# Optimization experiments

Measured on AMD Instinct MI355X. Metric: run time of the kernel, lower is better.

The kernel has to match this reference:

```python
import jax, jax.numpy as jnp
import numpy as np

EMBED = 1024
HEADS = 16
HEAD_DIM = EMBED // HEADS


def setup_inputs() -> dict:
    key = jax.random.key(0)
    ks = jax.random.split(key, 9)
    s = 1.0 / np.sqrt(EMBED)
    inp = {
        "x": jax.random.normal(ks[0], (2, 2048, EMBED), dtype=jnp.float32),
        "wq": jax.random.uniform(ks[1], (EMBED, EMBED), jnp.float32, -s, s),
        "bq": jax.random.uniform(ks[2], (EMBED,), jnp.float32, -s, s),
        "wk": jax.random.uniform(ks[3], (EMBED, EMBED), jnp.float32, -s, s),
        "bk": jax.random.uniform(ks[4], (EMBED,), jnp.float32, -s, s),
        "wv": jax.random.uniform(ks[5], (EMBED, EMBED), jnp.float32, -s, s),
        "bv": jax.random.uniform(ks[6], (EMBED,), jnp.float32, -s, s),
        "wo": jax.random.uniform(ks[7], (EMBED, EMBED), jnp.float32, -s, s),
        "bo": jax.random.uniform(ks[8], (EMBED,), jnp.float32, -s, s),
    }
    return inp


def reference(x, wq, bq, wk, bk, wv, bv, wo, bo):
    B, S, E = x.shape
    H, D = HEADS, HEAD_DIM
    # projections (torch Linear: y = x @ W.T + b; here weights stored as [E, E] applied as x @ W.T)
    q = (x @ wq.T + bq).reshape(B, S, H, D).transpose(0, 2, 1, 3)  # [B,H,S,D]
    k = (x @ wk.T + bk).reshape(B, S, H, D).transpose(0, 2, 1, 3)
    v = (x @ wv.T + bv).reshape(B, S, H, D).transpose(0, 2, 1, 3)
    scores = jnp.einsum("bhqd,bhkd->bhqk", q, k) / jnp.sqrt(jnp.asarray(D, x.dtype))
    attn = jax.nn.softmax(scores, axis=-1)  # dropout is identity in eval / p=0
    ctx = jnp.einsum("bhqk,bhkd->bhqd", attn, v)
    ctx = ctx.transpose(0, 2, 1, 3).reshape(B, S, E)
    return ctx @ wo.T + bo
```

## Files before the change

### kernel.cpp

```cpp
#include <hip/hip_runtime.h>
#include <hip/hip_bf16.h>

#define EMBED 1024
#define HEADS 16
#define HDIM  64
#define BATCH 2
#define SEQ   2048
#define MTOT  (BATCH*SEQ)

typedef __attribute__((ext_vector_type(8))) short bf16x8;
typedef __attribute__((ext_vector_type(4))) short bf16x4;
typedef __attribute__((ext_vector_type(4))) float f32x4;
typedef __attribute__((ext_vector_type(8))) unsigned short u16x8;
typedef __attribute__((ext_vector_type(2))) unsigned u32x2;
typedef __attribute__((ext_vector_type(4))) unsigned u32x4;

__device__ __forceinline__ unsigned pack2(float lo, float hi) {
    __hip_bfloat162 h = __float22bfloat162_rn(make_float2(lo, hi));
    unsigned u;
    __builtin_memcpy(&u, &h, sizeof(u));
    return u;
}
__device__ __forceinline__ unsigned short f2bf(float f) {
    __hip_bfloat16 h = __float2bfloat16(f);
    unsigned short u;
    __builtin_memcpy(&u, &h, sizeof(u));
    return u;
}

__device__ __forceinline__ f32x4 mfma16(bf16x4 a, bf16x4 b, f32x4 c) {
#if __has_builtin(__builtin_amdgcn_mfma_f32_16x16x16bf16_1k)
    return __builtin_amdgcn_mfma_f32_16x16x16bf16_1k(a, b, c, 0, 0, 0);
#else
    f32x4 d;
    asm volatile("v_mfma_f32_16x16x16_bf16 %0, %1, %2, %3"
                 : "=v"(d) : "v"(a), "v"(b), "v"(c));
    return d;
#endif
}

__device__ __forceinline__ void glds16(const void* g, void* l) {
    __builtin_amdgcn_global_load_lds(
        (const __attribute__((address_space(1))) void*)g,
        (__attribute__((address_space(3))) void*)l, 16, 0, 0);
}

__global__ __launch_bounds__(256) void preconvert(
    const float* __restrict__ x,
    const float* __restrict__ wq, const float* __restrict__ wk,
    const float* __restrict__ wv, const float* __restrict__ wo,
    unsigned short* __restrict__ xb,
    unsigned short* __restrict__ wqb, unsigned short* __restrict__ wkb,
    unsigned short* __restrict__ wvb, unsigned short* __restrict__ wob)
{
    const int NX = (MTOT * EMBED) / 4;
    const int NW = (EMBED * EMBED) / 4;
    int idx = blockIdx.x * 256 + threadIdx.x;
    const float* src;
    unsigned short* dst;
    int off;
    if (idx < NX) {
        src = x; dst = xb; off = idx;
    } else {
        int r = idx - NX;
        int w = r / NW;
        off = r - w * NW;
        src = (w == 0) ? wq : (w == 1) ? wk : (w == 2) ? wv : wo;
        dst = (w == 0) ? wqb : (w == 1) ? wkb : (w == 2) ? wvb : wob;
    }
    float4 v = ((const float4*)src)[off];
    u32x2 o;
    o[0] = pack2(v.x, v.y);
    o[1] = pack2(v.z, v.w);
    *(u32x2*)(dst + (size_t)off * 4) = o;
}

__global__ __launch_bounds__(256, 2) void qkv_proj(
    const unsigned short* __restrict__ xb,
    const unsigned short* __restrict__ wqb, const float* __restrict__ bq,
    const unsigned short* __restrict__ wkb, const float* __restrict__ bk,
    const unsigned short* __restrict__ wvb, const float* __restrict__ bv,
    unsigned short* __restrict__ qo,
    unsigned short* __restrict__ ko,
    unsigned short* __restrict__ vto)
{
    const int which = blockIdx.z;
    const unsigned short* __restrict__ w =
        (which == 0) ? wqb : (which == 1) ? wkb : wvb;
    const float* __restrict__ bias = (which == 0) ? bq : (which == 1) ? bk : bv;
    const float kscale = (which == 1) ? 0.18033688f : 1.0f;

    const int m0 = blockIdx.x * 128;
    const int n0 = blockIdx.y * 128;

    __shared__ __align__(16) unsigned short a_lds[128 * 32];
    __shared__ __align__(16) unsigned short b_lds[128 * 32];

    const int tid  = threadIdx.x;
    const int lane = tid & 63;
    const int wid  = tid >> 6;
    const int wr   = wid >> 1, wc = wid & 1;
    const int lq   = lane & 15;
    const int lg   = lane >> 4;

    f32x4 acc[4][4] = {};

    const int srow  = wid * 32 + (lane >> 2);
    const int scol8 = (lane & 3) * 8;
    const unsigned short* ap0 = xb + (size_t)(m0 + srow)      * EMBED + scol8;
    const unsigned short* ap1 = xb + (size_t)(m0 + srow + 16) * EMBED + scol8;
    const unsigned short* bp0 = w  + (size_t)(n0 + srow)      * EMBED + scol8;
    const unsigned short* bp1 = w  + (size_t)(n0 + srow + 16) * EMBED + scol8;
    unsigned short* la0 = a_lds + wid * 1024;
    unsigned short* la1 = a_lds + wid * 1024 + 512;
    unsigned short* lb0 = b_lds + wid * 1024;
    unsigned short* lb1 = b_lds + wid * 1024 + 512;

    for (int k0 = 0; k0 < EMBED; k0 += 32) {
        glds16(ap0 + k0, la0);
        glds16(ap1 + k0, la1);
        glds16(bp0 + k0, lb0);
        glds16(bp1 + k0, lb1);
        __syncthreads();
        bf16x8 af[4], bfr[4];
        #pragma unroll
        for (int i = 0; i < 4; ++i)
            af[i] = *(const bf16x8*)&a_lds[(wr*64 + i*16 + lq) * 32 + lg*8];
        #pragma unroll
        for (int j = 0; j < 4; ++j)
            bfr[j] = *(const bf16x8*)&b_lds[(wc*64 + j*16 + lq) * 32 + lg*8];
        #pragma unroll
        for (int i = 0; i < 4; ++i)
            #pragma unroll
            for (int j = 0; j < 4; ++j)
                acc[i][j] = __builtin_amdgcn_mfma_f32_16x16x32_bf16(af[i], bfr[j], acc[i][j], 0, 0, 0);
        __syncthreads();
    }

    #pragma unroll
    for (int j = 0; j < 4; ++j) {
        const int nn = n0 + wc*64 + j*16 + lq;
        const float bsv = bias[nn];
        const int h = nn >> 6, d = nn & (HDIM-1);
        #pragma unroll
        for (int i = 0; i < 4; ++i) {
            const int mmb = m0 + wr*64 + i*16 + lg*4;
            const int b = mmb >> 11;
            const int s = mmb & (SEQ-1);
            const size_t bh = (size_t)(b*HEADS + h);
            if (which == 2) {
                u32x2 ov;
                ov[0] = pack2(acc[i][j][0] + bsv, acc[i][j][1] + bsv);
                ov[1] = pack2(acc[i][j][2] + bsv, acc[i][j][3] + bsv);
                *(u32x2*)&vto[(bh*HDIM + d)*SEQ + s] = ov;
            } else {
                unsigned short* o = (which == 0) ? qo : ko;
                #pragma unroll
                for (int r = 0; r < 4; ++r)
                    o[(bh*SEQ + (s + r))*HDIM + d] = f2bf((acc[i][j][r] + bsv) * kscale);
            }
        }
    }
}

__global__ __launch_bounds__(256, 4) void attn(
    const unsigned short* __restrict__ q,
    const unsigned short* __restrict__ k,
    const unsigned short* __restrict__ vt,
    unsigned short* __restrict__ ctx)
{
    __shared__ __align__(16) unsigned char sm[2 * 16384];

    const int bid   = blockIdx.x;
    const int xcd   = bid & 7;
    const int local = bid >> 3;
    const int bh    = xcd * 4 + (local >> 5);
    const int q0    = (local & 31) * 64;
    const int b     = bh >> 4;
    const int h     = bh & (HEADS - 1);
    const int tid   = threadIdx.x;
    const int wv    = tid >> 6;
    const int lane  = tid & 63;
    const int lq = lane & 15, lg = lane >> 4;

    const unsigned short* qb = q  + (size_t)bh * SEQ * HDIM;
    const unsigned short* kb = k  + (size_t)bh * SEQ * HDIM;
    const unsigned short* vb = vt + (size_t)bh * HDIM * SEQ;

    const int swz    = (lq & 7) << 4;
    const int kread0 = lq*128 + ((lg*16)      ^ swz);
    const int kread1 = lq*128 + ((lg*16 + 64) ^ swz);

    const int vrd0 = lq*128 + ((lg*32)      ^ swz);
    const int vrd1 = lq*128 + ((lg*32 + 16) ^ swz);

    const int wrow = tid >> 3;
    const int c8   = tid & 7;
    const int wswz = (wrow & 7) << 4;
    const int woff = wrow*128 + ((c8 * 16) ^ wswz);
    const int vin0 = (c8 & 1)*64 + (c8 >> 1)*8;
    const int woffV0 = wrow*128 + (vin0        ^ wswz);
    const int woffV1 = wrow*128 + ((vin0 + 32) ^ wswz);

    const int scol = c8 * 8;
    const unsigned short* kp = kb + (size_t)wrow * HDIM + scol;
    const unsigned short* vp = vb + (size_t)wrow * SEQ + scol;

    bf16x8 qf[2];
    #pragma unroll
    for (int hh = 0; hh < 2; ++hh)
        qf[hh] = *(const bf16x8*)(qb + (size_t)(q0 + wv*16 + lq) * HDIM + hh*32 + lg*8);

    f32x4 o[4] = {};
    float lr = 0.f;

    u16x8 kr0, kr1, vr0, vr1;

#define LOADT() do {                                                           \
    kr0 = *(const u16x8*)(kp);                                                 \
    kr1 = *(const u16x8*)(kp + 32*HDIM);                                       \
    vr0 = *(const u16x8*)(vp);                                                 \
    vr1 = *(const u16x8*)(vp + 32*SEQ);                                        \
} while (0)

#define WRITET(BF) do {                                                        \
    unsigned char* smb = sm + (BF)*16384;                                      \
    *(u16x8*)(smb +        woff) = kr0;                                        \
    *(u16x8*)(smb + 4096 + woff) = kr1;                                        \
    u32x4 t0 = __builtin_bit_cast(u32x4, vr0);                                 \
    u32x4 t1 = __builtin_bit_cast(u32x4, vr1);                                 \
    u32x2 hlf;                                                                 \
    hlf[0] = t0[0]; hlf[1] = t0[1];                                            \
    *(u32x2*)(smb +  8192 + woffV0) = hlf;                                     \
    hlf[0] = t0[2]; hlf[1] = t0[3];                                            \
    *(u32x2*)(smb +  8192 + woffV1) = hlf;                                     \
    hlf[0] = t1[0]; hlf[1] = t1[1];                                            \
    *(u32x2*)(smb + 12288 + woffV0) = hlf;                                     \
    hlf[0] = t1[2]; hlf[1] = t1[3];                                            \
    *(u32x2*)(smb + 12288 + woffV1) = hlf;                                     \
} while (0)

#define COMPUTE(BF) do {                                                       \
    const unsigned char* smb = sm + (BF)*16384;                                \
    f32x4 s_[4];                                                               \
    _Pragma("unroll")                                                          \
    for (int sub = 0; sub < 4; ++sub) {                                        \
        bf16x8 k0 = *(const bf16x8*)(smb + sub*2048 + kread0);                 \
        bf16x8 k1 = *(const bf16x8*)(smb + sub*2048 + kread1);                 \
        f32x4 z = {};                                                          \
        z = __builtin_amdgcn_mfma_f32_16x16x32_bf16(k0, qf[0], z, 0, 0, 0);    \
        z = __builtin_amdgcn_mfma_f32_16x16x32_bf16(k1, qf[1], z, 0, 0, 0);    \
        s_[sub] = z;                                                           \
    }                                                                          \
    bf16x4 pf[4];                                                              \
    float psum = 0.f;                                                          \
    _Pragma("unroll")                                                          \
    for (int sub = 0; sub < 4; ++sub) {                                        \
        f32x4 pv;                                                              \
        _Pragma("unroll")                                                      \
        for (int r = 0; r < 4; ++r) pv[r] = exp2f(s_[sub][r]);                 \
        psum += (pv[0] + pv[1]) + (pv[2] + pv[3]);                             \
        u32x2 pk;                                                              \
        pk[0] = pack2(pv[0], pv[1]);                                           \
        pk[1] = pack2(pv[2], pv[3]);                                           \
        pf[sub] = __builtin_bit_cast(bf16x4, pk);                              \
    }                                                                          \
    lr += psum;                                                                \
    _Pragma("unroll")                                                          \
    for (int i = 0; i < 4; ++i) {                                              \
        bf16x8 v01 = *(const bf16x8*)(smb + 8192 + i*2048 + vrd0);             \
        bf16x8 v23 = *(const bf16x8*)(smb + 8192 + i*2048 + vrd1);             \
        u32x4 a01 = __builtin_bit_cast(u32x4, v01);                            \
        u32x4 a23 = __builtin_bit_cast(u32x4, v23);                            \
        u32x2 hw;                                                              \
        hw[0] = a01[0]; hw[1] = a01[1];                                        \
        o[i] = mfma16(__builtin_bit_cast(bf16x4, hw), pf[0], o[i]);            \
        hw[0] = a01[2]; hw[1] = a01[3];                                        \
        o[i] = mfma16(__builtin_bit_cast(bf16x4, hw), pf[1], o[i]);            \
        hw[0] = a23[0]; hw[1] = a23[1];                                        \
        o[i] = mfma16(__builtin_bit_cast(bf16x4, hw), pf[2], o[i]);            \
        hw[0] = a23[2]; hw[1] = a23[3];                                        \
        o[i] = mfma16(__builtin_bit_cast(bf16x4, hw), pf[3], o[i]);            \
    }                                                                          \
} while (0)

    LOADT();
    WRITET(0);
    __syncthreads();
    kp += 64 * HDIM;
    vp += 64;

    for (int t2 = 0; t2 < 16; ++t2) {
        {
            const int t = 2 * t2;
            if (t < 31) LOADT();
            COMPUTE(0);
            if (t < 31) {
                WRITET(1);
                __syncthreads();
                kp += 64 * HDIM;
                vp += 64;
            }
        }
        {
            const int t = 2 * t2 + 1;
            if (t < 31) LOADT();
            COMPUTE(1);
            if (t < 31) {
                WRITET(0);
                __syncthreads();
                kp += 64 * HDIM;
                vp += 64;
            }
        }
    }

#undef LOADT
#undef WRITET
#undef COMPUTE

    float lm = lr + __shfl_xor(lr, 16);
    lm += __shfl_xor(lm, 32);
    const float inv = 1.0f / lm;
    unsigned short* cb = ctx + ((size_t)(b*SEQ + q0 + wv*16 + lq)) * EMBED + h*HDIM;
    #pragma unroll
    for (int i = 0; i < 4; ++i) {
        u32x2 ov;
        ov[0] = pack2(o[i][0] * inv, o[i][1] * inv);
        ov[1] = pack2(o[i][2] * inv, o[i][3] * inv);
        *(u32x2*)(cb + i*16 + lg*4) = ov;
    }
}

__global__ __launch_bounds__(256, 2) void out_proj(
    const unsigned short* __restrict__ ctx,
    const unsigned short* __restrict__ wob, const float* __restrict__ bo,
    float* __restrict__ out)
{
    const int m0 = blockIdx.x * 128;
    const int n0 = blockIdx.y * 128;

    __shared__ __align__(16) unsigned short a_lds[128 * 32];
    __shared__ __align__(16) unsigned short b_lds[128 * 32];

    const int tid  = threadIdx.x;
    const int lane = tid & 63;
    const int wid  = tid >> 6;
    const int wr   = wid >> 1, wc = wid & 1;
    const int lq   = lane & 15;
    const int lg   = lane >> 4;

    f32x4 acc[4][4] = {};

    const int srow  = wid * 32 + (lane >> 2);
    const int scol8 = (lane & 3) * 8;
    const unsigned short* ap0 = ctx + (size_t)(m0 + srow)      * EMBED + scol8;
    const unsigned short* ap1 = ctx + (size_t)(m0 + srow + 16) * EMBED + scol8;
    const unsigned short* bp0 = wob + (size_t)(n0 + srow)      * EMBED + scol8;
    const unsigned short* bp1 = wob + (size_t)(n0 + srow + 16) * EMBED + scol8;
    unsigned short* la0 = a_lds + wid * 1024;
    unsigned short* la1 = a_lds + wid * 1024 + 512;
    unsigned short* lb0 = b_lds + wid * 1024;
    unsigned short* lb1 = b_lds + wid * 1024 + 512;

    for (int k0 = 0; k0 < EMBED; k0 += 32) {
        glds16(ap0 + k0, la0);
        glds16(ap1 + k0, la1);
        glds16(bp0 + k0, lb0);
        glds16(bp1 + k0, lb1);
        __syncthreads();
        bf16x8 af[4], bfr[4];
        #pragma unroll
        for (int i = 0; i < 4; ++i)
            af[i] = *(const bf16x8*)&a_lds[(wr*64 + i*16 + lq) * 32 + lg*8];
        #pragma unroll
        for (int j = 0; j < 4; ++j)
            bfr[j] = *(const bf16x8*)&b_lds[(wc*64 + j*16 + lq) * 32 + lg*8];
        #pragma unroll
        for (int i = 0; i < 4; ++i)
            #pragma unroll
            for (int j = 0; j < 4; ++j)
                acc[i][j] = __builtin_amdgcn_mfma_f32_16x16x32_bf16(af[i], bfr[j], acc[i][j], 0, 0, 0);
        __syncthreads();
    }

    #pragma unroll
    for (int j = 0; j < 4; ++j) {
        const int nn = n0 + wc*64 + j*16 + lq;
        const float bsv = bo[nn];
        #pragma unroll
        for (int i = 0; i < 4; ++i) {
            const int mm = m0 + wr*64 + i*16 + lg*4;
            #pragma unroll
            for (int r = 0; r < 4; ++r)
                out[(size_t)(mm + r) * EMBED + nn] = acc[i][j][r] + bsv;
        }
    }
}

extern "C" void kernel_launch(void* const* d_in, const int* in_sizes, int n_in,
                              void* d_out, int out_size, void* d_ws, size_t ws_size,
                              hipStream_t stream) {
    const float* x  = (const float*)d_in[0];
    const float* wq = (const float*)d_in[1];
    const float* bq = (const float*)d_in[2];
    const float* wk = (const float*)d_in[3];
    const float* bk = (const float*)d_in[4];
    const float* wv = (const float*)d_in[5];
    const float* bv = (const float*)d_in[6];
    const float* wo = (const float*)d_in[7];
    const float* bo = (const float*)d_in[8];
    float* out = (float*)d_out;

    const size_t NELEM = (size_t)MTOT * EMBED;
    const size_t WELEM = (size_t)EMBED * EMBED;
    unsigned short* q_ws   = (unsigned short*)d_ws;
    unsigned short* k_ws   = q_ws  + NELEM;
    unsigned short* vt_ws  = k_ws  + NELEM;
    unsigned short* ctx_ws = vt_ws + NELEM;
    unsigned short* wqb    = ctx_ws + NELEM;
    unsigned short* wkb    = wqb + WELEM;
    unsigned short* wvb    = wkb + WELEM;
    unsigned short* wob    = wvb + WELEM;
    unsigned short* xb     = ctx_ws;

    const int NCONV = (int)((NELEM + 4 * WELEM) / 4);
    preconvert<<<dim3(NCONV / 256), 256, 0, stream>>>(
        x, wq, wk, wv, wo, xb, wqb, wkb, wvb, wob);
    qkv_proj<<<dim3(MTOT/128, EMBED/128, 3), 256, 0, stream>>>(
        xb, wqb, bq, wkb, bk, wvb, bv, q_ws, k_ws, vt_ws);
    attn<<<dim3(SEQ/64 * BATCH*HEADS), 256, 0, stream>>>(q_ws, k_ws, vt_ws, ctx_ws);
    out_proj<<<dim3(MTOT/128, EMBED/128), 256, 0, stream>>>(ctx_ws, wob, bo, out);
}
```

Before: 139.0 us.

## Use 16x16x32 MFMA for PV product with remapped K/V LDS layout

Replaces the four 16x16x16 bf16 MFMAs per output tile in the P·V product with two 16x16x32 MFMAs. To do that, the row mapping of K reads changes so that the score registers line up with the larger k-dimension operand, and the LDS swizzle for K and V is redesigned. V tiles are now written to LDS as full 16-byte stores instead of split 8-byte halves. This is meant to cut MFMA issue count, the register shuffling of P fragments, and LDS write instructions, at the cost of a trickier index permutation that must stay bank-conflict free and correct.

New measurement: 134.8 us. 1.03x faster.

```diff
diff --git a/kernel.cpp b/kernel.cpp
--- a/kernel.cpp
+++ b/kernel.cpp
@@ -26,17 +26,6 @@
     unsigned short u;
     __builtin_memcpy(&u, &h, sizeof(u));
     return u;
-}
-
-__device__ __forceinline__ f32x4 mfma16(bf16x4 a, bf16x4 b, f32x4 c) {
-#if __has_builtin(__builtin_amdgcn_mfma_f32_16x16x16bf16_1k)
-    return __builtin_amdgcn_mfma_f32_16x16x16bf16_1k(a, b, c, 0, 0, 0);
-#else
-    f32x4 d;
-    asm volatile("v_mfma_f32_16x16x16_bf16 %0, %1, %2, %3"
-                 : "=v"(d) : "v"(a), "v"(b), "v"(c));
-    return d;
-#endif
 }
 
 __device__ __forceinline__ void glds16(const void* g, void* l) {
@@ -187,20 +176,18 @@
     const unsigned short* kb = k  + (size_t)bh * SEQ * HDIM;
     const unsigned short* vb = vt + (size_t)bh * HDIM * SEQ;
 
-    const int swz    = (lq & 7) << 4;
-    const int kread0 = lq*128 + ((lg*16)      ^ swz);
-    const int kread1 = lq*128 + ((lg*16 + 64) ^ swz);
-
-    const int vrd0 = lq*128 + ((lg*32)      ^ swz);
-    const int vrd1 = lq*128 + ((lg*32 + 16) ^ swz);
+    const int lg16 = lg * 16;
+    const int Sp = (((lq & 3) | (((lq >> 2) & 1) << 2)) << 4);
+    const int Tp = (((lq & 3) | (((lq >> 3) & 1) << 2)) << 4);
+    const int kreadA = (8*(lq >> 2) + (lq & 3)) * 128 + (lg16 ^ Sp);
+    const int kreadB = kreadA ^ 64;
+    const int vreadA = lq * 128 + (lg16 ^ Tp);
+    const int vreadB = vreadA ^ 64;
 
     const int wrow = tid >> 3;
     const int c8   = tid & 7;
-    const int wswz = (wrow & 7) << 4;
-    const int woff = wrow*128 + ((c8 * 16) ^ wswz);
-    const int vin0 = (c8 & 1)*64 + (c8 >> 1)*8;
-    const int woffV0 = wrow*128 + (vin0        ^ wswz);
-    const int woffV1 = wrow*128 + ((vin0 + 32) ^ wswz);
+    const int wS   = (((wrow & 3) | (((wrow >> 3) & 1) << 2)) << 4);
+    const int woff = wrow * 128 + ((c8 * 16) ^ wS);
 
     const int scol = c8 * 8;
     const unsigned short* kp = kb + (size_t)wrow * HDIM + scol;
@@ -225,19 +212,10 @@
 
 #define WRITET(BF) do {                                                        \
     unsigned char* smb = sm + (BF)*16384;                                      \
-    *(u16x8*)(smb +        woff) = kr0;                                        \
-    *(u16x8*)(smb + 4096 + woff) = kr1;                                        \
-    u32x4 t0 = __builtin_bit_cast(u32x4, vr0);                                 \
-    u32x4 t1 = __builtin_bit_cast(u32x4, vr1);                                 \
-    u32x2 hlf;                                                                 \
-    hlf[0] = t0[0]; hlf[1] = t0[1];                                            \
-    *(u32x2*)(smb +  8192 + woffV0) = hlf;                                     \
-    hlf[0] = t0[2]; hlf[1] = t0[3];                                            \
-    *(u32x2*)(smb +  8192 + woffV1) = hlf;                                     \
-    hlf[0] = t1[0]; hlf[1] = t1[1];                                            \
-    *(u32x2*)(smb + 12288 + woffV0) = hlf;                                     \
-    hlf[0] = t1[2]; hlf[1] = t1[3];                                            \
-    *(u32x2*)(smb + 12288 + woffV1) = hlf;                                     \
+    *(u16x8*)(smb +         woff) = kr0;                                       \
+    *(u16x8*)(smb +  4096 + woff) = kr1;                                       \
+    *(u16x8*)(smb +  8192 + woff) = vr0;                                       \
+    *(u16x8*)(smb + 12288 + woff) = vr1;                                       \
 } while (0)
 
 #define COMPUTE(BF) do {                                                       \
@@ -245,14 +223,15 @@
     f32x4 s_[4];                                                               \
     _Pragma("unroll")                                                          \
     for (int sub = 0; sub < 4; ++sub) {                                        \
-        bf16x8 k0 = *(const bf16x8*)(smb + sub*2048 + kread0);                 \
-        bf16x8 k1 = *(const bf16x8*)(smb + sub*2048 + kread1);                 \
+        const int sadd = (sub & 1) * 512 + (sub >> 1) * 4096;                  \
+        bf16x8 k0 = *(const bf16x8*)(smb + sadd + kreadA);                     \
+        bf16x8 k1 = *(const bf16x8*)(smb + sadd + kreadB);                     \
         f32x4 z = {};                                                          \
         z = __builtin_amdgcn_mfma_f32_16x16x32_bf16(k0, qf[0], z, 0, 0, 0);    \
         z = __builtin_amdgcn_mfma_f32_16x16x32_bf16(k1, qf[1], z, 0, 0, 0);    \
         s_[sub] = z;                                                           \
     }                                                                          \
-    bf16x4 pf[4];                                                              \
+    u32x4 pbw0, pbw1;                                                          \
     float psum = 0.f;                                                          \
     _Pragma("unroll")                                                          \
     for (int sub = 0; sub < 4; ++sub) {                                        \
@@ -260,27 +239,22 @@
         _Pragma("unroll")                                                      \
         for (int r = 0; r < 4; ++r) pv[r] = exp2f(s_[sub][r]);                 \
         psum += (pv[0] + pv[1]) + (pv[2] + pv[3]);                             \
-        u32x2 pk;                                                              \
-        pk[0] = pack2(pv[0], pv[1]);                                           \
-        pk[1] = pack2(pv[2], pv[3]);                                           \
-        pf[sub] = __builtin_bit_cast(bf16x4, pk);                              \
+        unsigned d0 = pack2(pv[0], pv[1]);                                     \
+        unsigned d1 = pack2(pv[2], pv[3]);                                     \
+        if (sub == 0)      { pbw0[0] = d0; pbw0[1] = d1; }                     \
+        else if (sub == 1) { pbw0[2] = d0; pbw0[3] = d1; }                     \
+        else if (sub == 2) { pbw1[0] = d0; pbw1[1] = d1; }                     \
+        else               { pbw1[2] = d0; pbw1[3] = d1; }                     \
     }                                                                          \
     lr += psum;                                                                \
+    bf16x8 pb0 = __builtin_bit_cast(bf16x8, pbw0);                             \
+    bf16x8 pb1 = __builtin_bit_cast(bf16x8, pbw1);                             \
     _Pragma("unroll")                                                          \
     for (int i = 0; i < 4; ++i) {                                              \
-        bf16x8 v01 = *(const bf16x8*)(smb + 8192 + i*2048 + vrd0);             \
-        bf16x8 v23 = *(const bf16x8*)(smb + 8192 + i*2048 + vrd1);             \
-        u32x4 a01 = __builtin_bit_cast(u32x4, v01);                            \
-        u32x4 a23 = __builtin_bit_cast(u32x4, v23);                            \
-        u32x2 hw;                                                              \
-        hw[0] = a01[0]; hw[1] = a01[1];                                        \
-        o[i] = mfma16(__builtin_bit_cast(bf16x4, hw), pf[0], o[i]);            \
-        hw[0] = a01[2]; hw[1] = a01[3];                                        \
-        o[i] = mfma16(__builtin_bit_cast(bf16x4, hw), pf[1], o[i]);            \
-        hw[0] = a23[0]; hw[1] = a23[1];                                        \
-        o[i] = mfma16(__builtin_bit_cast(bf16x4, hw), pf[2], o[i]);            \
-        hw[0] = a23[2]; hw[1] = a23[3];                                        \
-        o[i] = mfma16(__builtin_bit_cast(bf16x4, hw), pf[3], o[i]);            \
+        bf16x8 va = *(const bf16x8*)(smb + 8192 + i*2048 + vreadA);            \
+        bf16x8 vbq = *(const bf16x8*)(smb + 8192 + i*2048 + vreadB);           \
+        o[i] = __builtin_amdgcn_mfma_f32_16x16x32_bf16(va,  pb0, o[i], 0, 0, 0); \
+        o[i] = __builtin_amdgcn_mfma_f32_16x16x32_bf16(vbq, pb1, o[i], 0, 0, 0); \
     }                                                                          \
 } while (0)
 
```
